# Performance work log

Measured on AMD Instinct MI355X. Metric: run time of the kernel, lower is better.

Reference implementation:

```python
import jax, jax.numpy as jnp
import numpy as np

PATCH = 8

def _conv2d(x, w, b, groups=1, pad=0):
    out = jax.lax.conv_general_dilated(
        x, w, window_strides=(1, 1), padding=[(pad, pad), (pad, pad)],
        dimension_numbers=('NCHW', 'OIHW', 'NCHW'), feature_group_count=groups)
    return out + b[None, :, None, None]

def setup_inputs() -> dict:
    key = jax.random.key(0)
    ks = jax.random.split(key, 9)
    B, C, H, W = 8, 32, 256, 256
    C2 = 2 * C
    x = jax.random.normal(ks[0], (B, C, H, W), jnp.float32)
    w_in = jax.random.normal(ks[1], (C2, C, 1, 1), jnp.float32) * 0.1
    b_in = jax.random.normal(ks[2], (C2,), jnp.float32) * 0.01
    fft1 = 1.0 + 0.1 * jax.random.normal(ks[3], (C2, 1, 1, PATCH, PATCH // 2 + 1), jnp.float32)
    fft2 = 1.0 + 0.1 * jax.random.normal(ks[4], (C2, 1, 1, PATCH, PATCH // 2 + 1), jnp.float32)
    w_dw = jax.random.normal(ks[5], (C2, 1, 7, 7), jnp.float32) * 0.05
    b_dw = jax.random.normal(ks[6], (C2,), jnp.float32) * 0.01
    w_out = jax.random.normal(ks[7], (C, C2, 1, 1), jnp.float32) * 0.1
    b_out = jax.random.normal(ks[8], (C,), jnp.float32) * 0.01
    return {'x': x, 'w_in': w_in, 'b_in': b_in, 'fft1': fft1, 'fft2': fft2,
            'w_dw': w_dw, 'b_dw': b_dw, 'w_out': w_out, 'b_out': b_out}

def reference(x, w_in, b_in, fft1, fft2, w_dw, b_dw, w_out, b_out):
    B, C, H, W = x.shape
    C2 = 2 * C
    # 1x1 conv in: C -> 2C
    x = _conv2d(x, w_in, b_in)
    # rearrange b c (h p1) (w p2) -> b c h w p1 p2
    Hp, Wp = H // PATCH, W // PATCH
    xp = x.reshape(B, C2, Hp, PATCH, Wp, PATCH).transpose(0, 1, 2, 4, 3, 5)
    # per-patch 2D rFFT (norm='backward' = default) and learnable spectral filter
    f = jnp.fft.rfft2(xp.astype(jnp.float32)) * fft1  # [B,C2,Hp,Wp,8,5] complex
    y = jax.nn.gelu(jnp.concatenate([f.real, f.imag], axis=1), approximate=False)
    yr, yi = jnp.split(y, 2, axis=1)
    f2 = jax.lax.complex(yr, yi) * fft2
    xp = jnp.fft.irfft2(f2, s=(PATCH, PATCH))  # [B,C2,Hp,Wp,8,8]
    x = xp.transpose(0, 1, 2, 4, 3, 5).reshape(B, C2, H, W)
    # 7x7 depthwise conv + GELU + 1x1 conv out: 2C -> C
    x = _conv2d(x, w_dw, b_dw, groups=C2, pad=3)
    x = jax.nn.gelu(x, approximate=False)
    x = _conv2d(x, w_out, b_out)
    return x
```

## Files before the change

kernel.cpp:

```cpp
#include <hip/hip_runtime.h>
#include <math.h>

#define C_IN 32
#define C2C 64
#define HH 256
#define WW 256

#define R2 0.70710678118654752f

__device__ __forceinline__ float gelu_f(float x) {
    float u = x * R2;
    float a = fabsf(u);
    float t = __builtin_amdgcn_rcpf(fmaf(0.3275911f, a, 1.0f));
    float p = t * fmaf(t, fmaf(t, fmaf(t, fmaf(t, 1.061405429f, -1.453152027f),
                                       1.421413741f), -0.284496736f), 0.254829592f);
    float e = __expf(-a * a);
    float er = fmaf(-p, e, 1.0f);
    er = copysignf(er, u);
    return 0.5f * x * (1.0f + er);
}

__device__ const float CT8d[8] = {1.0f, R2, 0.0f, -R2, -1.0f, -R2, 0.0f, R2};
__device__ const float ST8d[8] = {0.0f, R2, 1.0f, R2, 0.0f, -R2, -1.0f, -R2};

__device__ __forceinline__ void rdft8(const float t[8], float Ar[5], float Ai[5]) {
    float e0 = t[0] + t[4], e1 = t[1] + t[5], e2 = t[2] + t[6], e3 = t[3] + t[7];
    float s04 = t[0] - t[4], s26 = t[2] - t[6];
    float am = t[1] - t[3] - t[5] + t[7];
    float bm = t[1] + t[3] - t[5] - t[7];
    float e02 = e0 + e2, e13 = e1 + e3;
    Ar[0] = e02 + e13;
    Ar[4] = e02 - e13;
    Ar[2] = e0 - e2;
    Ai[2] = e3 - e1;
    float ma = R2 * am, mb = R2 * bm;
    Ar[1] = s04 + ma;
    Ar[3] = s04 - ma;
    Ai[1] = -s26 - mb;
    Ai[3] = s26 - mb;
    Ai[0] = 0.f;
    Ai[4] = 0.f;
}

__device__ __forceinline__ void wrA5(float* ubuf, int c2x, int l,
                                     const float Ar[5], const float Ai[5]) {
    float* pr = &ubuf[c2x * 44 + l];
    float* pi = &ubuf[2816 + c2x * 44 + l];
    pr[0]  = Ar[0];  pi[0]  = 0.f;
    pr[8]  = Ar[1];  pi[8]  = Ai[1];
    pr[16] = Ar[2];  pi[16] = Ai[2];
    pr[24] = Ar[3];  pi[24] = Ai[3];
    pr[32] = Ar[4];  pi[32] = 0.f;
}

__device__ __forceinline__ void colpass(const float* ubuf, int c2x, int l,
                                        const float* __restrict__ fft1,
                                        const float* __restrict__ fft2,
                                        float gr[5], float gi[5]) {
    constexpr float CT[8] = {1.0f, R2, 0.0f, -R2, -1.0f, -R2, 0.0f, R2};
    constexpr float ST[8] = {0.0f, R2, 1.0f, R2, 0.0f, -R2, -1.0f, -R2};
    const int row = (l <= 4) ? l : 8 - l;
    const float sgn = (l <= 4) ? 1.0f : -1.0f;
    float Ar2[8], Ai2[8];
    {
        const float4 r0 = *(const float4*)&ubuf[c2x * 44 + row * 8];
        const float4 r1 = *(const float4*)&ubuf[c2x * 44 + row * 8 + 4];
        const float4 i0 = *(const float4*)&ubuf[2816 + c2x * 44 + row * 8];
        const float4 i1 = *(const float4*)&ubuf[2816 + c2x * 44 + row * 8 + 4];
        Ar2[0] = r0.x; Ar2[1] = r0.y; Ar2[2] = r0.z; Ar2[3] = r0.w;
        Ar2[4] = r1.x; Ar2[5] = r1.y; Ar2[6] = r1.z; Ar2[7] = r1.w;
        Ai2[0] = sgn * i0.x; Ai2[1] = sgn * i0.y; Ai2[2] = sgn * i0.z; Ai2[3] = sgn * i0.w;
        Ai2[4] = sgn * i1.x; Ai2[5] = sgn * i1.y; Ai2[6] = sgn * i1.z; Ai2[7] = sgn * i1.w;
    }
    #pragma unroll
    for (int v = 0; v < 5; ++v) {
        float fr = 0.f, fi = 0.f;
        #pragma unroll
        for (int w = 0; w < 8; ++w) {
            const int k = (v * w) & 7;
            fr += Ar2[w] * CT[k] + Ai2[w] * ST[k];
            fi += Ai2[w] * CT[k] - Ar2[w] * ST[k];
        }
        const float s1 = fft1[(c2x * 8 + l) * 5 + v];
        const float s2 = fft2[(c2x * 8 + l) * 5 + v];
        gr[v] = gelu_f(fr * s1) * s2;
        gi[v] = gelu_f(fi * s1) * s2;
    }
}

__device__ __forceinline__ void invpass(const float* gtab, float c1, float s1, float o[8]) {
    constexpr float CT[8] = {1.0f, R2, 0.0f, -R2, -1.0f, -R2, 0.0f, R2};
    constexpr float ST[8] = {0.0f, R2, 1.0f, R2, 0.0f, -R2, -1.0f, -R2};
    float Rr[5] = {0.f, 0.f, 0.f, 0.f, 0.f};
    float Ri[5] = {0.f, 0.f, 0.f, 0.f, 0.f};
    float cu = 1.f, su = 0.f;
    #pragma unroll
    for (int u = 0; u < 8; ++u) {
        const float4 g0 = *(const float4*)&gtab[u * 12];
        const float4 g1 = *(const float4*)&gtab[u * 12 + 4];
        const float2 g2 = *(const float2*)&gtab[u * 12 + 8];
        Rr[0] += g0.x * cu - g0.y * su;  Ri[0] += g0.x * su + g0.y * cu;
        Rr[1] += g0.z * cu - g0.w * su;  Ri[1] += g0.z * su + g0.w * cu;
        Rr[2] += g1.x * cu - g1.y * su;  Ri[2] += g1.x * su + g1.y * cu;
        Rr[3] += g1.z * cu - g1.w * su;  Ri[3] += g1.z * su + g1.w * cu;
        Rr[4] += g2.x * cu - g2.y * su;  Ri[4] += g2.x * su + g2.y * cu;
        const float nc = cu * c1 - su * s1;
        su = cu * s1 + su * c1;
        cu = nc;
    }
    #pragma unroll
    for (int w = 0; w < 8; ++w) {
        float s = 0.f;
        #pragma unroll
        for (int v = 0; v < 5; ++v) {
            const float m = (v == 0 || v == 4) ? 1.0f : 2.0f;
            const int k = (v * w) & 7;
            s += m * (Rr[v] * CT[k] - Ri[v] * ST[k]);
        }
        o[w] = s * 0.015625f;
    }
}

__global__ __launch_bounds__(256, 4)
void k1_spectral(const float* __restrict__ x, const float* __restrict__ w_in,
                 const float* __restrict__ b_in, const float* __restrict__ fft1,
                 const float* __restrict__ fft2, float* __restrict__ z)
{
    __shared__ __align__(16) float ubuf[6400];

    const int tid = threadIdx.x;
    const int c2 = tid >> 3;
    const int l  = tid & 7;

    int Lf = blockIdx.x + (blockIdx.y << 5) + (blockIdx.z << 10);
    int Lp = ((Lf & 7) << 10) | (Lf >> 3);
    const int b  = Lp >> 10;
    const int hp = (Lp >> 5) & 31;
    const int wp = Lp & 31;
    const int h0 = hp << 3, w0 = wp << 3;

    #pragma unroll
    for (int k = 0; k < 2; ++k) {
        int i = tid + (k << 8);
        int c = i >> 4, rem = i & 15;
        int h = rem >> 1, half = rem & 1;
        const float4 v = *(const float4*)&x[((b * C_IN + c) * HH + h0 + h) * WW + w0 + (half << 2)];
        int base = c * 100 + half * 48 + h;
        ubuf[base]      = v.x;
        ubuf[base + 12] = v.y;
        ubuf[base + 24] = v.z;
        ubuf[base + 36] = v.w;
    }
    #pragma unroll
    for (int k = 0; k < 2; ++k) {
        int i = tid + (k << 8);
        int ci = i >> 3, c4 = (i & 7) << 2;
        const float4 v = *(const float4*)&w_in[ci * C_IN + c4];
        int col = ((ci & 31) << 1) | (ci >> 5);
        ubuf[3200 + (c4 + 0) * 66 + col] = v.x;
        ubuf[3200 + (c4 + 1) * 66 + col] = v.y;
        ubuf[3200 + (c4 + 2) * 66 + col] = v.z;
        ubuf[3200 + (c4 + 3) * 66 + col] = v.w;
    }
    __syncthreads();

    float t0[8], t1[8];
    {
        const float bv0 = b_in[c2], bv1 = b_in[c2 + 32];
        #pragma unroll
        for (int h = 0; h < 8; ++h) { t0[h] = bv0; t1[h] = bv1; }
        #pragma unroll
        for (int c = 0; c < C_IN; ++c) {
            const float2 wv = *(const float2*)&ubuf[3200 + c * 66 + (c2 << 1)];
            const float4 xa = *(const float4*)&ubuf[c * 100 + l * 12];
            const float4 xb = *(const float4*)&ubuf[c * 100 + l * 12 + 4];
            float xv[8];
            xv[0] = xa.x; xv[1] = xa.y; xv[2] = xa.z; xv[3] = xa.w;
            xv[4] = xb.x; xv[5] = xb.y; xv[6] = xb.z; xv[7] = xb.w;
            #pragma unroll
            for (int h = 0; h < 8; ++h) {
                t0[h] = fmaf(wv.x, xv[h], t0[h]);
                t1[h] = fmaf(wv.y, xv[h], t1[h]);
            }
        }
    }

    float Ar_a[5], Ai_a[5], Ar_b[5], Ai_b[5];
    rdft8(t0, Ar_a, Ai_a);
    rdft8(t1, Ar_b, Ai_b);
    __syncthreads();
    wrA5(ubuf, c2,      l, Ar_a, Ai_a);
    wrA5(ubuf, c2 + 32, l, Ar_b, Ai_b);
    __syncthreads();

    float gr_a[5], gi_a[5], gr_b[5], gi_b[5];
    colpass(ubuf, c2,      l, fft1, fft2, gr_a, gi_a);
    colpass(ubuf, c2 + 32, l, fft1, fft2, gr_b, gi_b);
    __syncthreads();
    {
        int gb = c2 * 100 + l * 12;
        *(float4*)&ubuf[gb]     = make_float4(gr_a[0], gi_a[0], gr_a[1], gi_a[1]);
        *(float4*)&ubuf[gb + 4] = make_float4(gr_a[2], gi_a[2], gr_a[3], gi_a[3]);
        *(float2*)&ubuf[gb + 8] = make_float2(gr_a[4], gi_a[4]);
        gb = (c2 + 32) * 100 + l * 12;
        *(float4*)&ubuf[gb]     = make_float4(gr_b[0], gi_b[0], gr_b[1], gi_b[1]);
        *(float4*)&ubuf[gb + 4] = make_float4(gr_b[2], gi_b[2], gr_b[3], gi_b[3]);
        *(float2*)&ubuf[gb + 8] = make_float2(gr_b[4], gi_b[4]);
    }
    __syncthreads();

    const float c1 = CT8d[l], s1 = ST8d[l];
    float o[8];
    invpass(&ubuf[c2 * 100], c1, s1, o);
    {
        float* zp = &z[((b * C2C + c2) * HH + h0 + l) * WW + w0];
        *(float4*)&zp[0] = make_float4(o[0], o[1], o[2], o[3]);
        *(float4*)&zp[4] = make_float4(o[4], o[5], o[6], o[7]);
    }
    invpass(&ubuf[(c2 + 32) * 100], c1, s1, o);
    {
        float* zp = &z[((b * C2C + c2 + 32) * HH + h0 + l) * WW + w0];
        *(float4*)&zp[0] = make_float4(o[0], o[1], o[2], o[3]);
        *(float4*)&zp[4] = make_float4(o[4], o[5], o[6], o[7]);
    }
}

__global__ __launch_bounds__(256, 4)
void k2_dwconv(const float* __restrict__ z, const float* __restrict__ w_dw,
               const float* __restrict__ b_dw, const float* __restrict__ w_out,
               const float* __restrict__ b_out, float* __restrict__ out)
{
    __shared__ __align__(16) float zs[4 * 22 * 24];
    __shared__ __align__(16) float gbuf[4 * 16 * 24];

    const int tid = threadIdx.x;

    int L = blockIdx.x + (blockIdx.y << 4) + (blockIdx.z << 8);
    int Lp = ((L & 7) << 8) | (L >> 3);
    const int b  = Lp >> 8;
    const int ty = (Lp >> 4) & 15;
    const int tx = Lp & 15;
    const int x0g = tx << 4, y0g = ty << 4;

    const int lane = tid & 63;
    const int wv   = tid >> 6;
    const int bx   = lane & 3;
    const int oy   = lane >> 2;

    const int ox = tid & 15, py = tid >> 4;

    float acc[32];
    #pragma unroll
    for (int c = 0; c < 32; ++c) acc[c] = b_out[c];

    for (int chunk = 0; chunk < 16; ++chunk) {
        const int cbase = chunk << 2;
        __syncthreads();

        for (int i = tid; i < 528; i += 256) {
            int c2l = i / 132;
            int r   = i - c2l * 132;
            int yy  = r / 6;
            int x4  = r - yy * 6;
            int gy = y0g - 3 + yy;
            int gx = x0g - 4 + (x4 << 2);
            float4 v = make_float4(0.f, 0.f, 0.f, 0.f);
            if ((unsigned)gy < HH && (unsigned)gx < WW)
                v = *(const float4*)&z[((b * C2C + cbase + c2l) * HH + gy) * WW + gx];
            *(float4*)&zs[c2l * 528 + yy * 24 + (x4 << 2)] = v;
        }
        __syncthreads();

        {
            const int c2u = __builtin_amdgcn_readfirstlane(cbase + wv);
            const float* wd = &w_dw[c2u * 49];
            const float bd = b_dw[c2u];
            float a0 = bd, a1 = bd, a2 = bd, a3 = bd;
            const float* zb = &zs[wv * 528 + oy * 24 + (bx << 2)];
            #pragma unroll
            for (int ky = 0; ky < 7; ++ky) {
                const float4 q0 = *(const float4*)&zb[ky * 24];
                const float4 q1 = *(const float4*)&zb[ky * 24 + 4];
                const float4 q2 = *(const float4*)&zb[ky * 24 + 8];
                const float fv[11] = {q0.x, q0.y, q0.z, q0.w, q1.x, q1.y, q1.z, q1.w,
                                      q2.x, q2.y, q2.z};
                #pragma unroll
                for (int kx = 0; kx < 7; ++kx) {
                    const float w = wd[ky * 7 + kx];
                    a0 = fmaf(w, fv[kx + 1], a0);
                    a1 = fmaf(w, fv[kx + 2], a1);
                    a2 = fmaf(w, fv[kx + 3], a2);
                    a3 = fmaf(w, fv[kx + 4], a3);
                }
            }
            *(float4*)&gbuf[wv * 384 + oy * 24 + (bx << 2)] =
                make_float4(gelu_f(a0), gelu_f(a1), gelu_f(a2), gelu_f(a3));
        }
        __syncthreads();

        #pragma unroll
        for (int cc = 0; cc < 4; ++cc) {
            const float gv = gbuf[cc * 384 + py * 24 + ox];
            const int c2i = cbase + cc;
            #pragma unroll
            for (int c = 0; c < 32; ++c)
                acc[c] = fmaf(w_out[c * C2C + c2i], gv, acc[c]);
        }
    }

    #pragma unroll
    for (int c = 0; c < 32; ++c)
        out[((b * C_IN + c) * HH + y0g + py) * WW + x0g + ox] = acc[c];
}

extern "C" void kernel_launch(void* const* d_in, const int* in_sizes, int n_in,
                              void* d_out, int out_size, void* d_ws, size_t ws_size,
                              hipStream_t stream) {
    const float* x     = (const float*)d_in[0];
    const float* w_in  = (const float*)d_in[1];
    const float* b_in  = (const float*)d_in[2];
    const float* fft1  = (const float*)d_in[3];
    const float* fft2  = (const float*)d_in[4];
    const float* w_dw  = (const float*)d_in[5];
    const float* b_dw  = (const float*)d_in[6];
    const float* w_out = (const float*)d_in[7];
    const float* b_out = (const float*)d_in[8];
    float* outp = (float*)d_out;
    float* z = (float*)d_ws;

    dim3 g1(32, 32, 8);
    k1_spectral<<<g1, 256, 0, stream>>>(x, w_in, b_in, fft1, fft2, z);
    dim3 g2(16, 16, 8);
    k2_dwconv<<<g2, 256, 0, stream>>>(z, w_dw, b_dw, w_out, b_out, outp);
}
```

Before: 401.2 us.

## Store intermediate in patch-contiguous layout and XOR-swizzle dwconv shared memory

The spectral kernel now writes its output in a patch-major layout (each 8x8 patch contiguous), so each thread's stores form a contiguous 256-byte block per patch. The depthwise-conv kernel reads that layout back with remapped addressing. It also pads its shared tiles to a 32-float stride with an XOR swizzle and reassigns lanes (oy fastest) to reduce LDS bank conflicts. Launch bounds are raised to 6 waves per SIMD, which constrains registers and may cause spills in k2's 32-accumulator loop.

```diff
diff --git a/kernel.cpp b/kernel.cpp
--- a/kernel.cpp
+++ b/kernel.cpp
@@ -121,7 +121,7 @@
     }
 }
 
-__global__ __launch_bounds__(256, 4)
+__global__ __launch_bounds__(256, 6)
 void k1_spectral(const float* __restrict__ x, const float* __restrict__ w_in,
                  const float* __restrict__ b_in, const float* __restrict__ fft1,
                  const float* __restrict__ fft2, float* __restrict__ z)
@@ -211,27 +211,28 @@
 
     const float c1 = CT8d[l], s1 = ST8d[l];
     float o[8];
+    const int pbase = (((b * C2C) * 1024) + hp * 32 + wp) << 6;
     invpass(&ubuf[c2 * 100], c1, s1, o);
     {
-        float* zp = &z[((b * C2C + c2) * HH + h0 + l) * WW + w0];
+        float* zp = &z[pbase + (c2 << 16) + (l << 3)];
         *(float4*)&zp[0] = make_float4(o[0], o[1], o[2], o[3]);
         *(float4*)&zp[4] = make_float4(o[4], o[5], o[6], o[7]);
     }
     invpass(&ubuf[(c2 + 32) * 100], c1, s1, o);
     {
-        float* zp = &z[((b * C2C + c2 + 32) * HH + h0 + l) * WW + w0];
+        float* zp = &z[pbase + ((c2 + 32) << 16) + (l << 3)];
         *(float4*)&zp[0] = make_float4(o[0], o[1], o[2], o[3]);
         *(float4*)&zp[4] = make_float4(o[4], o[5], o[6], o[7]);
     }
 }
 
-__global__ __launch_bounds__(256, 4)
+__global__ __launch_bounds__(256, 6)
 void k2_dwconv(const float* __restrict__ z, const float* __restrict__ w_dw,
                const float* __restrict__ b_dw, const float* __restrict__ w_out,
                const float* __restrict__ b_out, float* __restrict__ out)
 {
-    __shared__ __align__(16) float zs[4 * 22 * 24];
-    __shared__ __align__(16) float gbuf[4 * 16 * 24];
+    __shared__ __align__(16) float zs[4 * 22 * 32];
+    __shared__ __align__(16) float gbuf[4 * 16 * 32];
 
     const int tid = threadIdx.x;
 
@@ -244,8 +245,8 @@
 
     const int lane = tid & 63;
     const int wv   = tid >> 6;
-    const int bx   = lane & 3;
-    const int oy   = lane >> 2;
+    const int bx   = lane >> 4;
+    const int oy   = lane & 15;
 
     const int ox = tid & 15, py = tid >> 4;
 
@@ -265,9 +266,12 @@
             int gy = y0g - 3 + yy;
             int gx = x0g - 4 + (x4 << 2);
             float4 v = make_float4(0.f, 0.f, 0.f, 0.f);
-            if ((unsigned)gy < HH && (unsigned)gx < WW)
-                v = *(const float4*)&z[((b * C2C + cbase + c2l) * HH + gy) * WW + gx];
-            *(float4*)&zs[c2l * 528 + yy * 24 + (x4 << 2)] = v;
+            if ((unsigned)gy < HH && (unsigned)gx < WW) {
+                const int hp = gy >> 3, wpp = gx >> 3;
+                const int off = ((gy & 7) << 3) | (gx & 7);
+                v = *(const float4*)&z[(((b * C2C + cbase + c2l) * 1024 + hp * 32 + wpp) << 6) + off];
+            }
+            *(float4*)&zs[c2l * 704 + yy * 32 + ((x4 ^ (yy & 7)) << 2)] = v;
         }
         __syncthreads();
 
@@ -276,12 +280,15 @@
             const float* wd = &w_dw[c2u * 49];
             const float bd = b_dw[c2u];
             float a0 = bd, a1 = bd, a2 = bd, a3 = bd;
-            const float* zb = &zs[wv * 528 + oy * 24 + (bx << 2)];
+            const float* zch = &zs[wv * 704];
             #pragma unroll
             for (int ky = 0; ky < 7; ++ky) {
-                const float4 q0 = *(const float4*)&zb[ky * 24];
-                const float4 q1 = *(const float4*)&zb[ky * 24 + 4];
-                const float4 q2 = *(const float4*)&zb[ky * 24 + 8];
+                const int row = oy + ky;
+                const int rs = row & 7;
+                const float* zr = &zch[row * 32];
+                const float4 q0 = *(const float4*)&zr[((bx ^ rs) << 2)];
+                const float4 q1 = *(const float4*)&zr[(((bx + 1) ^ rs) << 2)];
+                const float4 q2 = *(const float4*)&zr[(((bx + 2) ^ rs) << 2)];
                 const float fv[11] = {q0.x, q0.y, q0.z, q0.w, q1.x, q1.y, q1.z, q1.w,
                                       q2.x, q2.y, q2.z};
                 #pragma unroll
@@ -293,18 +300,21 @@
                     a3 = fmaf(w, fv[kx + 4], a3);
                 }
             }
-            *(float4*)&gbuf[wv * 384 + oy * 24 + (bx << 2)] =
+            *(float4*)&gbuf[wv * 512 + oy * 32 + ((bx ^ (oy & 7)) << 2)] =
                 make_float4(gelu_f(a0), gelu_f(a1), gelu_f(a2), gelu_f(a3));
         }
         __syncthreads();
 
-        #pragma unroll
-        for (int cc = 0; cc < 4; ++cc) {
-            const float gv = gbuf[cc * 384 + py * 24 + ox];
-            const int c2i = cbase + cc;
+        {
+            const int sw = (((ox >> 2) ^ (py & 7)) << 2) | (ox & 3);
             #pragma unroll
-            for (int c = 0; c < 32; ++c)
-                acc[c] = fmaf(w_out[c * C2C + c2i], gv, acc[c]);
+            for (int cc = 0; cc < 4; ++cc) {
+                const float gv = gbuf[cc * 512 + py * 32 + sw];
+                const int c2i = cbase + cc;
+                #pragma unroll
+                for (int c = 0; c < 32; ++c)
+                    acc[c] = fmaf(w_out[c * C2C + c2i], gv, acc[c]);
+            }
         }
     }
 
```

Result: slower. 749.0 us (+86.7%).
